# Kernel optimization log

Measured on AMD Instinct MI355X. Metric: run time of the kernel, lower is better.

The kernel has to match this reference:

```python
import jax, jax.numpy as jnp
import numpy as np

EMBED = 1024
HEADS = 16
HEAD_DIM = EMBED // HEADS
HIDDEN = 4 * EMBED
EPS = 1e-5


def layer_norm(x, g, b):
    mu = jnp.mean(x, axis=-1, keepdims=True)
    var = jnp.var(x, axis=-1, keepdims=True)
    return (x - mu) * jax.lax.rsqrt(var + EPS) * g + b


def setup_inputs() -> dict:
    key = jax.random.key(0)
    ks = jax.random.split(key, 12)
    s_e = 1.0 / np.sqrt(EMBED)
    s_h = 1.0 / np.sqrt(HIDDEN)
    return {
        "x": jax.random.normal(ks[0], (8, 1024, EMBED), dtype=jnp.float32),
        "ln1_g": jnp.ones((EMBED,), jnp.float32),
        "ln1_b": jnp.zeros((EMBED,), jnp.float32),
        "w_qkv": jax.random.normal(ks[1], (EMBED, 3 * EMBED), jnp.float32) * s_e,
        "b_qkv": jax.random.normal(ks[2], (3 * EMBED,), jnp.float32) * s_e,
        "w_out": jax.random.normal(ks[3], (EMBED, EMBED), jnp.float32) * s_e,
        "b_out": jax.random.normal(ks[4], (EMBED,), jnp.float32) * s_e,
        "ln2_g": jnp.ones((EMBED,), jnp.float32),
        "ln2_b": jnp.zeros((EMBED,), jnp.float32),
        "w_up": jax.random.normal(ks[5], (EMBED, HIDDEN), jnp.float32) * s_e,
        "b_up": jax.random.normal(ks[6], (HIDDEN,), jnp.float32) * s_e,
        "w_down": jax.random.normal(ks[7], (HIDDEN, EMBED), jnp.float32) * s_h,
        "b_down": jax.random.normal(ks[8], (EMBED,), jnp.float32) * s_h,
    }


def reference(x, ln1_g, ln1_b, w_qkv, b_qkv, w_out, b_out,
              ln2_g, ln2_b, w_up, b_up, w_down, b_down):
    B, T, C = x.shape
    # --- attention sub-block ---
    h = layer_norm(x, ln1_g, ln1_b)
    qkv = h @ w_qkv + b_qkv                                   # [B,T,3C]
    q, k, v = jnp.split(qkv, 3, axis=-1)
    def heads(t):  # [B,T,C] -> [B,H,T,D]
        return t.reshape(B, T, HEADS, HEAD_DIM).transpose(0, 2, 1, 3)
    q, k, v = heads(q), heads(k), heads(v)
    scale = HEAD_DIM ** -0.5
    attn = jax.nn.softmax(jnp.einsum('bhqd,bhkd->bhqk', q, k) * scale, axis=-1)
    y = jnp.einsum('bhqk,bhkd->bhqd', attn, v)                # [B,H,T,D]
    y = y.transpose(0, 2, 1, 3).reshape(B, T, C)
    x = x + y @ w_out + b_out
    # --- MLP sub-block ---
    h = layer_norm(x, ln2_g, ln2_b)
    h = jax.nn.relu(h @ w_up + b_up)
    x = x + h @ w_down + b_down
    return x
```

## Files before the change

### kernel.cpp

```cpp
#include <hip/hip_runtime.h>
#include <stdint.h>


typedef __attribute__((ext_vector_type(8))) short short8;
typedef __attribute__((ext_vector_type(4))) short short4v;
typedef __attribute__((ext_vector_type(4))) float floatx4;

#define NROWS 8192

__device__ __forceinline__ unsigned short f2bf(float f) {
    union { float f; unsigned u; } x; x.f = f;
    unsigned r = x.u + 0x7fffu + ((x.u >> 16) & 1u);
    return (unsigned short)(r >> 16);
}
__device__ __forceinline__ float bf2f(unsigned short h) {
    union { unsigned u; float f; } x; x.u = (unsigned)h << 16; return x.f;
}

__device__ __forceinline__ void gl2lds16(const unsigned short* g, unsigned short* l) {
    __builtin_amdgcn_global_load_lds(
        (const __attribute__((address_space(1))) unsigned int*)(uintptr_t)g,
        (__attribute__((address_space(3))) unsigned int*)(unsigned int)(uintptr_t)l,
        16, 0, 0);
}

__global__ __launch_bounds__(256) void prep_kernel(
    const float* __restrict__ w_qkv, const float* __restrict__ w_out,
    const float* __restrict__ w_up, const float* __restrict__ w_down,
    unsigned short* __restrict__ wqkvT, unsigned short* __restrict__ woutT,
    unsigned short* __restrict__ wupT, unsigned short* __restrict__ wdownT,
    const float* __restrict__ x, const float* __restrict__ g,
    const float* __restrict__ b, unsigned short* __restrict__ h1)
{
    int bid = blockIdx.x;
    if (bid < 3072) {
        __shared__ unsigned short tile[64][65];
        const float* in; unsigned short* out; int K, N, tb;
        if (bid < 768)       { in = w_qkv;  out = wqkvT;  K = 1024; N = 3072; tb = bid; }
        else if (bid < 1024) { in = w_out;  out = woutT;  K = 1024; N = 1024; tb = bid - 768; }
        else if (bid < 2048) { in = w_up;   out = wupT;   K = 1024; N = 4096; tb = bid - 1024; }
        else                 { in = w_down; out = wdownT; K = 4096; N = 1024; tb = bid - 2048; }
        int ntb = N >> 6;
        int n0 = (tb % ntb) * 64, k0 = (tb / ntb) * 64;
        int t = threadIdx.x;
        int ty = t >> 4, tx = t & 15;
        #pragma unroll
        for (int i = 0; i < 4; ++i) {
            float4 v = *(const float4*)&in[(size_t)(k0 + ty + 16 * i) * N + n0 + 4 * tx];
            tile[ty + 16 * i][4 * tx + 0] = f2bf(v.x);
            tile[ty + 16 * i][4 * tx + 1] = f2bf(v.y);
            tile[ty + 16 * i][4 * tx + 2] = f2bf(v.z);
            tile[ty + 16 * i][4 * tx + 3] = f2bf(v.w);
        }
        __syncthreads();
        int wy = t >> 3, wx = t & 7;
        #pragma unroll
        for (int i = 0; i < 2; ++i) {
            int n = wy + 32 * i;
            ushort4 lo, hi;
            lo.x = tile[8 * wx + 0][n]; lo.y = tile[8 * wx + 1][n];
            lo.z = tile[8 * wx + 2][n]; lo.w = tile[8 * wx + 3][n];
            hi.x = tile[8 * wx + 4][n]; hi.y = tile[8 * wx + 5][n];
            hi.z = tile[8 * wx + 6][n]; hi.w = tile[8 * wx + 7][n];
            unsigned short* dst = &out[(size_t)(n0 + n) * K + k0 + 8 * wx];
            *(ushort4*)dst = lo;
            *(ushort4*)(dst + 4) = hi;
        }
    } else {
        __shared__ float rs[4], rs2[4];
        int row = bid - 3072, t = threadIdx.x;
        const float4* xr = (const float4*)(x + (size_t)row * 1024);
        float4 v = xr[t];
        float s  = v.x + v.y + v.z + v.w;
        float s2 = v.x * v.x + v.y * v.y + v.z * v.z + v.w * v.w;
        #pragma unroll
        for (int off = 32; off; off >>= 1) {
            s  += __shfl_xor(s,  off, 64);
            s2 += __shfl_xor(s2, off, 64);
        }
        int w = t >> 6;
        if ((t & 63) == 0) { rs[w] = s; rs2[w] = s2; }
        __syncthreads();
        s  = rs[0] + rs[1] + rs[2] + rs[3];
        s2 = rs2[0] + rs2[1] + rs2[2] + rs2[3];
        float mean = s * (1.0f / 1024.0f);
        float var  = s2 * (1.0f / 1024.0f) - mean * mean;
        float rstd = rsqrtf(var + 1e-5f);
        float4 gv = ((const float4*)g)[t];
        float4 bv = ((const float4*)b)[t];
        ushort4 o;
        o.x = f2bf((v.x - mean) * rstd * gv.x + bv.x);
        o.y = f2bf((v.y - mean) * rstd * gv.y + bv.y);
        o.z = f2bf((v.z - mean) * rstd * gv.z + bv.z);
        o.w = f2bf((v.w - mean) * rstd * gv.w + bv.w);
        ((ushort4*)(h1 + (size_t)row * 1024))[t] = o;
    }
}

__global__ __launch_bounds__(256) void ln_bf16b(
    const unsigned short* __restrict__ x, const float* __restrict__ g,
    const float* __restrict__ b, unsigned short* __restrict__ out)
{
    int row = blockIdx.x, t = threadIdx.x;
    ushort4 hv = ((const ushort4*)(x + (size_t)row * 1024))[t];
    float v0 = bf2f(hv.x), v1 = bf2f(hv.y), v2 = bf2f(hv.z), v3 = bf2f(hv.w);
    float s  = v0 + v1 + v2 + v3;
    float s2 = v0 * v0 + v1 * v1 + v2 * v2 + v3 * v3;
    #pragma unroll
    for (int off = 32; off; off >>= 1) {
        s  += __shfl_xor(s,  off, 64);
        s2 += __shfl_xor(s2, off, 64);
    }
    __shared__ float rs[4], rs2[4];
    int w = t >> 6;
    if ((t & 63) == 0) { rs[w] = s; rs2[w] = s2; }
    __syncthreads();
    s  = rs[0] + rs[1] + rs[2] + rs[3];
    s2 = rs2[0] + rs2[1] + rs2[2] + rs2[3];
    float mean = s * (1.0f / 1024.0f);
    float var  = s2 * (1.0f / 1024.0f) - mean * mean;
    float rstd = rsqrtf(var + 1e-5f);
    float4 gv = ((const float4*)g)[t];
    float4 bv = ((const float4*)b)[t];
    ushort4 o;
    o.x = f2bf((v0 - mean) * rstd * gv.x + bv.x);
    o.y = f2bf((v1 - mean) * rstd * gv.y + bv.y);
    o.z = f2bf((v2 - mean) * rstd * gv.z + bv.z);
    o.w = f2bf((v3 - mean) * rstd * gv.w + bv.w);
    ((ushort4*)(out + (size_t)row * 1024))[t] = o;
}

template <int MODE>
__global__ __launch_bounds__(512, 2) void gemm_8ph(
    const unsigned short* __restrict__ A, const unsigned short* __restrict__ Bt,
    int M, int N, int K,
    const float* __restrict__ bias,
    unsigned short* __restrict__ outB)
{
    int m0 = blockIdx.x * 256, n0 = blockIdx.y * 256;
    int tid = threadIdx.x;
    int w = tid >> 6, l = tid & 63, quad = l >> 4, lr = l & 15;
    int wm = w >> 2, wn = w & 3;

    __shared__ unsigned short As[2][256 * 64];
    __shared__ unsigned short Bs[2][256 * 64];

    floatx4 acc[8][4];
    #pragma unroll
    for (int i = 0; i < 8; ++i)
        #pragma unroll
        for (int j = 0; j < 4; ++j)
            acc[i][j] = (floatx4){0.f, 0.f, 0.f, 0.f};

    int srow = l >> 3;
    int swz  = ((l & 7) ^ srow) * 8;
    int arow1 = (w < 4) ? 16 * w : 128 + 16 * (w - 4);
    const unsigned short* Ag = A  + (size_t)(m0 + arow1 + srow) * K + swz;
    const unsigned short* Bg = Bt + (size_t)(n0 + 16 * w + srow) * K + swz;
    int nt = K >> 6;

    auto SB = [&](unsigned short* dst, int h, int kt) {
        #pragma unroll
        for (int u = 0; u < 2; ++u)
            gl2lds16(Bg + (size_t)(128 * h + 8 * u) * K + kt * 64,
                     &dst[(128 * h + 16 * w + 8 * u) * 64]);
    };
    auto SA1 = [&](unsigned short* dst, int kt) {
        #pragma unroll
        for (int u = 0; u < 2; ++u)
            gl2lds16(Ag + (size_t)(8 * u) * K + kt * 64,
                     &dst[(arow1 + 8 * u) * 64]);
    };
    auto SA2 = [&](unsigned short* dst, int kt) {
        #pragma unroll
        for (int u = 0; u < 2; ++u)
            gl2lds16(Ag + (size_t)(64 + 8 * u) * K + kt * 64,
                     &dst[(arow1 + 64 + 8 * u) * 64]);
    };

    SB(Bs[0], 0, 0); SB(Bs[0], 1, 0); SA1(As[0], 0); SA2(As[0], 0);
    SB(Bs[1], 0, 1); SB(Bs[1], 1, 1); SA1(As[1], 1);
    asm volatile("s_waitcnt vmcnt(6)" ::: "memory");
    __builtin_amdgcn_s_barrier();

    for (int t = 0; t < nt; ++t) {
        int b = t & 1;
        const unsigned short* Asb = As[b];
        const unsigned short* Bsb = Bs[b];
        short8 bfr[4][2];
        #pragma unroll
        for (int p = 0; p < 4; ++p) {
            if (p == 0) {
                #pragma unroll
                for (int j = 0; j < 4; ++j)
                    #pragma unroll
                    for (int s = 0; s < 2; ++s)
                        bfr[j][s] = *(const short8*)
                            &Bsb[(64 * wn + 16 * j + lr) * 64 +
                                 (((s * 4 + quad) ^ (lr & 7)) * 8)];
            }
            short8 af[2][2];
            #pragma unroll
            for (int i = 0; i < 2; ++i)
                #pragma unroll
                for (int s = 0; s < 2; ++s)
                    af[i][s] = *(const short8*)
                        &Asb[(128 * wm + 32 * p + 16 * i + lr) * 64 +
                             (((s * 4 + quad) ^ (lr & 7)) * 8)];
            if (p == 0) asm volatile("s_waitcnt lgkmcnt(8)" ::: "memory");

            if (p == 0)      { if (t + 1 < nt) SA2(As[b ^ 1], t + 1); }
            else if (p == 1) { if (t + 2 < nt) SB(Bs[b], 0, t + 2); }
            else if (p == 2) { if (t + 2 < nt) SB(Bs[b], 1, t + 2); }
            else             { if (t + 2 < nt) SA1(As[b], t + 2); }

            __builtin_amdgcn_s_barrier();
            asm volatile("s_waitcnt lgkmcnt(0)" ::: "memory");
            __builtin_amdgcn_s_setprio(1);
            #pragma unroll
            for (int i = 0; i < 2; ++i)
                #pragma unroll
                for (int j = 0; j < 4; ++j) {
                    acc[2 * p + i][j] = __builtin_amdgcn_mfma_f32_16x16x32_bf16(
                        af[i][0], bfr[j][0], acc[2 * p + i][j], 0, 0, 0);
                    acc[2 * p + i][j] = __builtin_amdgcn_mfma_f32_16x16x32_bf16(
                        af[i][1], bfr[j][1], acc[2 * p + i][j], 0, 0, 0);
                }
            __builtin_amdgcn_s_setprio(0);
            if (p == 3) {
                if (t + 2 >= nt) asm volatile("s_waitcnt vmcnt(0)" ::: "memory");
                else             asm volatile("s_waitcnt vmcnt(6)" ::: "memory");
            }
            __builtin_amdgcn_s_barrier();
        }
    }

    #pragma unroll
    for (int mi = 0; mi < 8; ++mi)
        #pragma unroll
        for (int j = 0; j < 4; ++j)
            #pragma unroll
            for (int r = 0; r < 4; ++r) {
                int m = m0 + 128 * wm + 16 * mi + quad * 4 + r;
                int n = n0 + 64 * wn + 16 * j + lr;
                outB[(size_t)m * N + n] = f2bf(fmaxf(acc[mi][j][r] + bias[n], 0.f));
            }
}

template <int MODE>
__global__ __launch_bounds__(512, 2) void gemm_bn128(
    const unsigned short* __restrict__ A, const unsigned short* __restrict__ Bt,
    int M, int N, int K,
    const float* __restrict__ bias,
    const float* __restrict__ residF, const unsigned short* __restrict__ residB,
    float* __restrict__ outF, unsigned short* __restrict__ outB,
    unsigned short* __restrict__ qO, unsigned short* __restrict__ kO,
    unsigned short* __restrict__ vO)
{
    int m0 = blockIdx.x * 256, n0 = blockIdx.y * 128;
    int tid = threadIdx.x;
    int w = tid >> 6, l = tid & 63, quad = l >> 4, lr = l & 15;
    int wm = w >> 1, wn = w & 1;

    __shared__ unsigned short As[2][256 * 64];
    __shared__ unsigned short Bs[2][128 * 64];

    floatx4 acc[4][4];
    #pragma unroll
    for (int i = 0; i < 4; ++i)
        #pragma unroll
        for (int j = 0; j < 4; ++j)
            acc[i][j] = (floatx4){0.f, 0.f, 0.f, 0.f};

    int srow = l >> 3;
    int swz  = ((l & 7) ^ srow) * 8;
    const unsigned short* Ag = A  + (size_t)(m0 + 16 * w + srow) * K + swz;
    const unsigned short* Bg = Bt + (size_t)(n0 + 16 * w + srow) * K + swz;
    int nt = K >> 6;

    auto SB = [&](unsigned short* dst, int kt) {
        #pragma unroll
        for (int u = 0; u < 2; ++u)
            gl2lds16(Bg + (size_t)(8 * u) * K + kt * 64,
                     &dst[(16 * w + 8 * u) * 64]);
    };
    auto SA1 = [&](unsigned short* dst, int kt) {
        #pragma unroll
        for (int u = 0; u < 2; ++u)
            gl2lds16(Ag + (size_t)(8 * u) * K + kt * 64,
                     &dst[(16 * w + 8 * u) * 64]);
    };
    auto SA2 = [&](unsigned short* dst, int kt) {
        #pragma unroll
        for (int u = 0; u < 2; ++u)
            gl2lds16(Ag + (size_t)(128 + 8 * u) * K + kt * 64,
                     &dst[(128 + 16 * w + 8 * u) * 64]);
    };

    SB(Bs[0], 0); SA1(As[0], 0); SA2(As[0], 0);
    SB(Bs[1], 1);
    asm volatile("s_waitcnt vmcnt(2)" ::: "memory");
    __builtin_amdgcn_s_barrier();

    for (int t = 0; t < nt; ++t) {
        int b = t & 1;
        const unsigned short* Asb = As[b];
        const unsigned short* Bsb = Bs[b];
        short8 bfr[4][2];
        #pragma unroll
        for (int p = 0; p < 2; ++p) {
            if (p == 0) { if (t + 1 < nt) { SA1(As[b ^ 1], t + 1); SA2(As[b ^ 1], t + 1); } }
            else        { if (t + 2 < nt) SB(Bs[b], t + 2); }

            if (p == 0) {
                #pragma unroll
                for (int j = 0; j < 4; ++j)
                    #pragma unroll
                    for (int s = 0; s < 2; ++s)
                        bfr[j][s] = *(const short8*)
                            &Bsb[(64 * wn + 16 * j + lr) * 64 +
                                 (((s * 4 + quad) ^ (lr & 7)) * 8)];
            }
            short8 af[2][2];
            #pragma unroll
            for (int i = 0; i < 2; ++i)
                #pragma unroll
                for (int s = 0; s < 2; ++s)
                    af[i][s] = *(const short8*)
                        &Asb[(64 * wm + 32 * p + 16 * i + lr) * 64 +
                             (((s * 4 + quad) ^ (lr & 7)) * 8)];

            __builtin_amdgcn_s_barrier();
            asm volatile("s_waitcnt lgkmcnt(0)" ::: "memory");
            __builtin_amdgcn_s_setprio(1);
            #pragma unroll
            for (int i = 0; i < 2; ++i)
                #pragma unroll
                for (int j = 0; j < 4; ++j) {
                    acc[2 * p + i][j] = __builtin_amdgcn_mfma_f32_16x16x32_bf16(
                        af[i][0], bfr[j][0], acc[2 * p + i][j], 0, 0, 0);
                    acc[2 * p + i][j] = __builtin_amdgcn_mfma_f32_16x16x32_bf16(
                        af[i][1], bfr[j][1], acc[2 * p + i][j], 0, 0, 0);
                }
            __builtin_amdgcn_s_setprio(0);
            if (p == 1) {
                if (t + 2 >= nt) asm volatile("s_waitcnt vmcnt(0)" ::: "memory");
                else             asm volatile("s_waitcnt vmcnt(2)" ::: "memory");
            }
            __builtin_amdgcn_s_barrier();
        }
    }

    if (MODE == 0) {
        int sel = (n0 + 64 * wn) >> 10;
        if (sel < 2) {
            const float qscale = (sel == 0) ? 0.125f : 1.0f;
            unsigned short* dst = (sel == 0) ? qO : kO;
            #pragma unroll
            for (int mi = 0; mi < 4; ++mi)
                #pragma unroll
                for (int j = 0; j < 4; ++j)
                    #pragma unroll
                    for (int r = 0; r < 4; ++r) {
                        int m = m0 + 64 * wm + 16 * mi + quad * 4 + r;
                        int n = n0 + 64 * wn + 16 * j + lr;
                        float c = (acc[mi][j][r] + bias[n]) * qscale;
                        int bb = m >> 10, tt = m & 1023;
                        int cc = n & 1023, hh = cc >> 6, d = cc & 63;
                        dst[(((size_t)(bb * 16 + hh)) * 1024 + tt) * 64 + d] = f2bf(c);
                    }
        } else {
            int bb = m0 >> 10;
            #pragma unroll
            for (int mi = 0; mi < 4; ++mi) {
                int t0 = (m0 & 1023) + 64 * wm + 16 * mi + quad * 4;
                #pragma unroll
                for (int j = 0; j < 4; ++j) {
                    int n = n0 + 64 * wn + 16 * j + lr;
                    int cc = n & 1023, hh = cc >> 6, d = cc & 63;
                    float bn = bias[n];
                    ushort4 pk;
                    pk.x = f2bf(acc[mi][j][0] + bn);
                    pk.y = f2bf(acc[mi][j][1] + bn);
                    pk.z = f2bf(acc[mi][j][2] + bn);
                    pk.w = f2bf(acc[mi][j][3] + bn);
                    *(ushort4*)&vO[((size_t)(bb * 16 + hh) * 64 + d) * 1024 + t0] = pk;
                }
            }
        }
    } else {
        #pragma unroll
        for (int mi = 0; mi < 4; ++mi)
            #pragma unroll
            for (int j = 0; j < 4; ++j)
                #pragma unroll
                for (int r = 0; r < 4; ++r) {
                    int m = m0 + 64 * wm + 16 * mi + quad * 4 + r;
                    int n = n0 + 64 * wn + 16 * j + lr;
                    float c = acc[mi][j][r] + bias[n];
                    if (MODE == 1)
                        outB[(size_t)m * N + n] = f2bf(c + residF[(size_t)m * N + n]);
                    else
                        outF[(size_t)m * N + n] = c + bf2f(residB[(size_t)m * N + n]);
                }
    }
}

__global__ __launch_bounds__(256, 3) void attn_kernel(
    const unsigned short* __restrict__ qg, const unsigned short* __restrict__ kg,
    const unsigned short* __restrict__ vtg, unsigned short* __restrict__ y)
{
    int bid = blockIdx.x;
    int bh = bid & 127, qt = bid >> 7;
    int b = bh >> 4, h = bh & 15;
    int tid = threadIdx.x;
    int w = tid >> 6, l = tid & 63, quad = l >> 4, lr = l & 15;

    __shared__ unsigned short Ks[2][64 * 64];
    __shared__ unsigned short Vs[2][64 * 64];
    __shared__ unsigned short Ps[4][32 * 68];

    int srow = l >> 3;
    int scol = ((l & 7) ^ srow) * 8;

    const unsigned short* kbase = kg  + (size_t)bh * 65536;
    const unsigned short* vbase = vtg + (size_t)bh * 65536;

    #pragma unroll
    for (int u = 0; u < 2; ++u) {
        gl2lds16(kbase + (size_t)(16 * w + 8 * u + srow) * 64 + scol,
                 &Ks[0][(16 * w + 8 * u) * 64]);
        gl2lds16(vbase + (size_t)(16 * w + 8 * u + srow) * 1024 + scol,
                 &Vs[0][(16 * w + 8 * u) * 64]);
    }

    const unsigned short* qbase = qg + (size_t)bh * 65536 + (size_t)(qt * 128 + 32 * w) * 64;
    short8 af[2][2];
    #pragma unroll
    for (int i = 0; i < 2; ++i)
        #pragma unroll
        for (int s = 0; s < 2; ++s)
            af[i][s] = *(const short8*)
                &qbase[(16 * i + lr) * 64 + (s * 4 + quad) * 8];

    __syncthreads();

    floatx4 o[2][4];
    float lsum[2][4];
    #pragma unroll
    for (int i = 0; i < 2; ++i)
        #pragma unroll
        for (int j = 0; j < 4; ++j) o[i][j] = (floatx4){0.f, 0.f, 0.f, 0.f};
    #pragma unroll
    for (int i = 0; i < 2; ++i)
        #pragma unroll
        for (int r = 0; r < 4; ++r) lsum[i][r] = 0.f;

    for (int kt = 0; kt < 16; ++kt) {
        int cur = kt & 1;
        if (kt + 1 < 16) {
            const unsigned short* kb = kbase + (size_t)((kt + 1) * 64) * 64;
            const unsigned short* vb = vbase + (size_t)((kt + 1) * 64);
            #pragma unroll
            for (int u = 0; u < 2; ++u) {
                gl2lds16(kb + (size_t)(16 * w + 8 * u + srow) * 64 + scol,
                         &Ks[cur ^ 1][(16 * w + 8 * u) * 64]);
                gl2lds16(vb + (size_t)(16 * w + 8 * u + srow) * 1024 + scol,
                         &Vs[cur ^ 1][(16 * w + 8 * u) * 64]);
            }
        }

        short8 kf[4][2];
        #pragma unroll
        for (int j = 0; j < 4; ++j)
            #pragma unroll
            for (int s = 0; s < 2; ++s)
                kf[j][s] = *(const short8*)
                    &Ks[cur][(16 * j + lr) * 64 + ((s * 4 + quad) ^ (lr & 7)) * 8];

        floatx4 s[2][4];
        #pragma unroll
        for (int i = 0; i < 2; ++i)
            #pragma unroll
            for (int j = 0; j < 4; ++j) {
                s[i][j] = (floatx4){0.f, 0.f, 0.f, 0.f};
                #pragma unroll
                for (int st = 0; st < 2; ++st)
                    s[i][j] = __builtin_amdgcn_mfma_f32_16x16x32_bf16(
                        af[i][st], kf[j][st], s[i][j], 0, 0, 0);
            }

        #pragma unroll
        for (int i = 0; i < 2; ++i)
            #pragma unroll
            for (int j = 0; j < 4; ++j)
                #pragma unroll
                for (int r = 0; r < 4; ++r) {
                    float p = __expf(s[i][j][r]);
                    lsum[i][r] += p;
                    Ps[w][(16 * i + quad * 4 + r) * 68 + 16 * j + lr] = f2bf(p);
                }

        asm volatile("s_waitcnt lgkmcnt(0)" ::: "memory");

        short8 vf[4][2];
        #pragma unroll
        for (int j = 0; j < 4; ++j)
            #pragma unroll
            for (int s = 0; s < 2; ++s)
                vf[j][s] = *(const short8*)
                    &Vs[cur][(16 * j + lr) * 64 + ((s * 4 + quad) ^ (lr & 7)) * 8];

        #pragma unroll
        for (int i = 0; i < 2; ++i)
            #pragma unroll
            for (int st = 0; st < 2; ++st) {
                short4v p0 = *(const short4v*)&Ps[w][(16 * i + lr) * 68 + st * 32 + quad * 8];
                short4v p1 = *(const short4v*)&Ps[w][(16 * i + lr) * 68 + st * 32 + quad * 8 + 4];
                short8 pf;
                #pragma unroll
                for (int e = 0; e < 4; ++e) { pf[e] = p0[e]; pf[e + 4] = p1[e]; }
                #pragma unroll
                for (int j = 0; j < 4; ++j)
                    o[i][j] = __builtin_amdgcn_mfma_f32_16x16x32_bf16(
                        pf, vf[j][st], o[i][j], 0, 0, 0);
            }
        __syncthreads();
    }

    #pragma unroll
    for (int off = 8; off; off >>= 1)
        #pragma unroll
        for (int i = 0; i < 2; ++i)
            #pragma unroll
            for (int r = 0; r < 4; ++r)
                lsum[i][r] += __shfl_xor(lsum[i][r], off, 64);
    float rinv[2][4];
    #pragma unroll
    for (int i = 0; i < 2; ++i)
        #pragma unroll
        for (int r = 0; r < 4; ++r) rinv[i][r] = 1.0f / lsum[i][r];

    #pragma unroll
    for (int i = 0; i < 2; ++i)
        #pragma unroll
        for (int j = 0; j < 4; ++j)
            #pragma unroll
            for (int r = 0; r < 4; ++r) {
                int trow = qt * 128 + 32 * w + 16 * i + quad * 4 + r;
                int col  = h * 64 + 16 * j + lr;
                y[((size_t)b * 1024 + trow) * 1024 + col] =
                    f2bf(o[i][j][r] * rinv[i][r]);
            }
}

extern "C" void kernel_launch(void* const* d_in, const int* in_sizes, int n_in,
                              void* d_out, int out_size, void* d_ws, size_t ws_size,
                              hipStream_t stream)
{
    const float* x      = (const float*)d_in[0];
    const float* ln1_g  = (const float*)d_in[1];
    const float* ln1_b  = (const float*)d_in[2];
    const float* w_qkv  = (const float*)d_in[3];
    const float* b_qkv  = (const float*)d_in[4];
    const float* w_out  = (const float*)d_in[5];
    const float* b_out  = (const float*)d_in[6];
    const float* ln2_g  = (const float*)d_in[7];
    const float* ln2_b  = (const float*)d_in[8];
    const float* w_up   = (const float*)d_in[9];
    const float* b_up   = (const float*)d_in[10];
    const float* w_down = (const float*)d_in[11];
    const float* b_down = (const float*)d_in[12];

    char* ws = (char*)d_ws;
    unsigned short* wqkvT  = (unsigned short*)(ws + 0);
    unsigned short* woutT  = (unsigned short*)(ws + 6291456);
    unsigned short* wupT   = (unsigned short*)(ws + 8388608);
    unsigned short* wdownT = (unsigned short*)(ws + 16777216);
    unsigned short* x2     = (unsigned short*)(ws + 25165824);
    unsigned short* h1     = (unsigned short*)(ws + 58720256);
    unsigned short* qb     = (unsigned short*)(ws + 75497472);
    unsigned short* kb     = (unsigned short*)(ws + 92274688);
    unsigned short* vtb    = (unsigned short*)(ws + 109051904);
    unsigned short* yb     = (unsigned short*)(ws + 125829120);
    unsigned short* a2     = (unsigned short*)(ws + 75497472);
    unsigned short* h2     = h1;

    prep_kernel<<<11264, 256, 0, stream>>>(
        w_qkv, w_out, w_up, w_down, wqkvT, woutT, wupT, wdownT,
        x, ln1_g, ln1_b, h1);

    gemm_bn128<0><<<dim3(NROWS / 256, 3072 / 128), 512, 0, stream>>>(
        h1, wqkvT, NROWS, 3072, 1024, b_qkv,
        nullptr, nullptr, nullptr, nullptr, qb, kb, vtb);

    attn_kernel<<<1024, 256, 0, stream>>>(qb, kb, vtb, yb);

    gemm_bn128<1><<<dim3(NROWS / 256, 1024 / 128), 512, 0, stream>>>(
        yb, woutT, NROWS, 1024, 1024, b_out,
        x, nullptr, nullptr, x2, nullptr, nullptr, nullptr);

    ln_bf16b<<<NROWS, 256, 0, stream>>>(x2, ln2_g, ln2_b, h2);

    gemm_8ph<2><<<dim3(NROWS / 256, 4096 / 256), 512, 0, stream>>>(
        h2, wupT, NROWS, 4096, 1024, b_up, a2);

    gemm_bn128<3><<<dim3(NROWS / 256, 1024 / 128), 512, 0, stream>>>(
        a2, wdownT, NROWS, 1024, 4096, b_down,
        nullptr, x2, (float*)d_out, nullptr, nullptr, nullptr, nullptr);
}
```

Measured before the change: 433.4 us.

## Add register-resident B-fragment GEMM for the down projection

Adds a new GEMM kernel for the K=4096 down projection. Each wave loads its B (weight) fragments straight from global memory into double-buffered registers, so only the A tile is staged through LDS. This removes the LDS traffic and footprint for B and changes the pipelining and wait-count scheme. In exchange it raises register pressure and relies on hand-tuned vmcnt waits that must match the outstanding load counts exactly. The old MODE 3 epilogue branch is dropped from gemm_bn128.

```diff
diff --git a/kernel.cpp b/kernel.cpp
--- a/kernel.cpp
+++ b/kernel.cpp
@@ -398,12 +398,122 @@
                     int m = m0 + 64 * wm + 16 * mi + quad * 4 + r;
                     int n = n0 + 64 * wn + 16 * j + lr;
                     float c = acc[mi][j][r] + bias[n];
-                    if (MODE == 1)
-                        outB[(size_t)m * N + n] = f2bf(c + residF[(size_t)m * N + n]);
-                    else
-                        outF[(size_t)m * N + n] = c + bf2f(residB[(size_t)m * N + n]);
+                    outB[(size_t)m * N + n] = f2bf(c + residF[(size_t)m * N + n]);
                 }
     }
+}
+
+__global__ __launch_bounds__(512, 2) void gemm_breg(
+    const unsigned short* __restrict__ A, const unsigned short* __restrict__ Bt,
+    int M, int N, int K,
+    const float* __restrict__ bias,
+    const unsigned short* __restrict__ residB,
+    float* __restrict__ outF)
+{
+    int m0 = blockIdx.x * 256, n0 = blockIdx.y * 128;
+    int tid = threadIdx.x;
+    int w = tid >> 6, l = tid & 63, quad = l >> 4, lr = l & 15;
+    int wm = w >> 1, wn = w & 1;
+
+    __shared__ unsigned short As[2][256 * 64];
+
+    floatx4 acc[4][4];
+    #pragma unroll
+    for (int i = 0; i < 4; ++i)
+        #pragma unroll
+        for (int j = 0; j < 4; ++j)
+            acc[i][j] = (floatx4){0.f, 0.f, 0.f, 0.f};
+
+    int srow = l >> 3;
+    int swz  = ((l & 7) ^ srow) * 8;
+    const unsigned short* Ag = A + (size_t)(m0 + 16 * w + srow) * K + swz;
+    const unsigned short* Bf = Bt + (size_t)(n0 + 64 * wn + lr) * K + quad * 8;
+    int nt = K >> 6;
+
+    auto SA1 = [&](unsigned short* dst, int kt) {
+        #pragma unroll
+        for (int u = 0; u < 2; ++u)
+            gl2lds16(Ag + (size_t)(8 * u) * K + kt * 64,
+                     &dst[(16 * w + 8 * u) * 64]);
+    };
+    auto SA2 = [&](unsigned short* dst, int kt) {
+        #pragma unroll
+        for (int u = 0; u < 2; ++u)
+            gl2lds16(Ag + (size_t)(128 + 8 * u) * K + kt * 64,
+                     &dst[(128 + 16 * w + 8 * u) * 64]);
+    };
+    auto LB = [&](short8* bank, int kt) {
+        #pragma unroll
+        for (int j = 0; j < 4; ++j)
+            #pragma unroll
+            for (int s = 0; s < 2; ++s)
+                bank[j * 2 + s] = *(const short8*)
+                    &Bf[(size_t)(16 * j) * K + kt * 64 + s * 32];
+    };
+
+    short8 brgA[8], brgB[8];
+
+    LB(brgA, 0);
+    if (nt > 1) LB(brgB, 1);
+    SA1(As[0], 0); SA2(As[0], 0);
+    if (nt > 1) { SA1(As[1], 1); SA2(As[1], 1); }
+    asm volatile("s_waitcnt vmcnt(4)" ::: "memory");
+    __builtin_amdgcn_s_barrier();
+
+    auto TILE = [&](int t, short8* bank) {
+        int b = t & 1;
+        const unsigned short* Asb = As[b];
+        #pragma unroll
+        for (int p = 0; p < 2; ++p) {
+            if (p == 0) { if (t + 1 < nt) { SA1(As[b ^ 1], t + 1); SA2(As[b ^ 1], t + 1); } }
+
+            short8 af[2][2];
+            #pragma unroll
+            for (int i = 0; i < 2; ++i)
+                #pragma unroll
+                for (int s = 0; s < 2; ++s)
+                    af[i][s] = *(const short8*)
+                        &Asb[(64 * wm + 32 * p + 16 * i + lr) * 64 +
+                             (((s * 4 + quad) ^ (lr & 7)) * 8)];
+
+            __builtin_amdgcn_s_barrier();
+            asm volatile("s_waitcnt lgkmcnt(0)" ::: "memory");
+            __builtin_amdgcn_s_setprio(1);
+            #pragma unroll
+            for (int i = 0; i < 2; ++i)
+                #pragma unroll
+                for (int j = 0; j < 4; ++j) {
+                    acc[2 * p + i][j] = __builtin_amdgcn_mfma_f32_16x16x32_bf16(
+                        af[i][0], bank[j * 2 + 0], acc[2 * p + i][j], 0, 0, 0);
+                    acc[2 * p + i][j] = __builtin_amdgcn_mfma_f32_16x16x32_bf16(
+                        af[i][1], bank[j * 2 + 1], acc[2 * p + i][j], 0, 0, 0);
+                }
+            __builtin_amdgcn_s_setprio(0);
+            if (p == 1) {
+                if (t + 2 < nt) LB(bank, t + 2);
+                if (t + 2 >= nt) asm volatile("s_waitcnt vmcnt(0)" ::: "memory");
+                else             asm volatile("s_waitcnt vmcnt(8)" ::: "memory");
+            }
+            __builtin_amdgcn_s_barrier();
+        }
+    };
+
+    for (int t = 0; t < nt; t += 2) {
+        TILE(t, brgA);
+        if (t + 1 < nt) TILE(t + 1, brgB);
+    }
+
+    #pragma unroll
+    for (int mi = 0; mi < 4; ++mi)
+        #pragma unroll
+        for (int j = 0; j < 4; ++j)
+            #pragma unroll
+            for (int r = 0; r < 4; ++r) {
+                int m = m0 + 64 * wm + 16 * mi + quad * 4 + r;
+                int n = n0 + 64 * wn + 16 * j + lr;
+                float c = acc[mi][j][r] + bias[n];
+                outF[(size_t)m * N + n] = c + bf2f(residB[(size_t)m * N + n]);
+            }
 }
 
 __global__ __launch_bounds__(256, 3) void attn_kernel(
@@ -605,7 +715,6 @@
     gemm_8ph<2><<<dim3(NROWS / 256, 4096 / 256), 512, 0, stream>>>(
         h2, wupT, NROWS, 4096, 1024, b_up, a2);
 
-    gemm_bn128<3><<<dim3(NROWS / 256, 1024 / 128), 512, 0, stream>>>(
-        a2, wdownT, NROWS, 1024, 4096, b_down,
-        nullptr, x2, (float*)d_out, nullptr, nullptr, nullptr, nullptr);
-}
+    gemm_breg<<<dim3(NROWS / 256, 1024 / 128), 512, 0, stream>>>(
+        a2, wdownT, NROWS, 1024, 4096, b_down, x2, (float*)d_out);
+}
```

After: 510.6 us. 17.8% more time.
